# Kernel optimization log

Measured on AMD Instinct MI355X. Metric: run time of the kernel, lower is better.

Reference implementation:

```python
import jax, jax.numpy as jnp
import numpy as np

NUM_NODES = 20000
NUM_EDGES = 65536
WIDTH = 64
EDGE_FEAT = 6
HIDDEN = 128


def setup_inputs() -> dict:
    key = jax.random.key(0)
    ks = jax.random.split(key, 6)
    x = jax.random.normal(ks[0], (NUM_NODES, WIDTH), dtype=jnp.float32)
    edge_attr = jax.random.normal(ks[1], (NUM_EDGES, EDGE_FEAT), dtype=jnp.float32)
    # weight-generating MLP params (the `nn` callable), fan-in scaled
    W1 = jax.random.normal(ks[2], (EDGE_FEAT, HIDDEN), dtype=jnp.float32) / np.sqrt(EDGE_FEAT)
    b1 = jnp.zeros((HIDDEN,), dtype=jnp.float32)
    W2 = jax.random.normal(ks[3], (HIDDEN, WIDTH * WIDTH), dtype=jnp.float32) / np.sqrt(HIDDEN)
    b2 = jnp.zeros((WIDTH * WIDTH,), dtype=jnp.float32)
    senders = jax.random.randint(ks[4], (NUM_EDGES,), 0, NUM_NODES)
    receivers = jax.random.randint(ks[5], (NUM_EDGES,), 0, NUM_NODES)
    return {"x": x, "edge_attr": edge_attr, "W1": W1, "b1": b1,
            "W2": W2, "b2": b2, "senders": senders, "receivers": receivers}


def reference(x, edge_attr, W1, b1, W2, b2, senders, receivers):
    n_segs, width = x.shape
    # nn(edge_attr): (E, width*width) edge-conditioned weights
    h = jax.nn.relu(edge_attr @ W1 + b1)
    weight = (h @ W2 + b2).reshape(-1, width, width)  # (E, w, w)
    # gather sender features, per-edge (1,w) @ (w,w) matmul -> (E, w)
    msgs = jnp.einsum('ew,ewv->ev', x[senders], weight)
    # scatter-sum messages into receiver nodes (aggr == 'sum')
    return jax.ops.segment_sum(msgs, receivers, num_segments=n_segs)
```

## Files before the change

### kernel.cpp

```cpp
#include <hip/hip_runtime.h>
#include <stdint.h>

typedef _Float16 f16;
typedef f16 f16x8 __attribute__((ext_vector_type(8)));
typedef float f32x4 __attribute__((ext_vector_type(4)));

#define NUM_NODES 20000
#define NUM_EDGES 65536
#define WIDTH 64
#define EDGE_FEAT 6
#define HIDDEN 128
#define BM 256
#define NCHUNK 129
#define XPAD 72

#define XH_HALFS (NUM_NODES * WIDTH)
#define XCONV_BLKS 625
#define W2G_HALFS (NCHUNK * 4096)
#define HT_HALFS ((size_t)NCHUNK * NUM_EDGES)
#define HBLKS (NUM_EDGES / 256)
#define OUT_FLOATS (NUM_NODES * WIDTH)
#define ZBLKS 313

__device__ __forceinline__ void gload_lds16(const f16* g, f16* l) {
  __builtin_amdgcn_global_load_lds(
      (const __attribute__((address_space(1))) unsigned int*)g,
      (__attribute__((address_space(3))) unsigned int*)l, 16, 0, 0);
}

__global__ __launch_bounds__(256) void prep_kernel(
    const float* __restrict__ x, const float* __restrict__ W2,
    const float* __restrict__ b2, const float* __restrict__ ea,
    const float* __restrict__ W1, const float* __restrict__ b1,
    f16* __restrict__ ws_h, float* __restrict__ out, int use_ht)
{
  f16* x_h = ws_h;
  f16* W2g = ws_h + XH_HALFS;
  f16* hT  = ws_h + XH_HALFS + W2G_HALFS;
  const int blk = blockIdx.x, tid = threadIdx.x;

  if (blk < NCHUNK) {
    __shared__ float row[4096];
    const int ki = blk;
    const float* srcrow;
    if (ki < HIDDEN) {
      const float4* src = (const float4*)(W2 + (size_t)ki * 4096);
      #pragma unroll
      for (int i = 0; i < 4; ++i) {
        float4 v = src[tid + 256 * i];
        *(float4*)&row[(tid + 256 * i) * 4] = v;
      }
      __syncthreads();
      srcrow = row;
    } else {
      srcrow = b2;
    }
    const int obase = tid * 16;
    f16x8 outv0, outv1;
    #pragma unroll
    for (int u = 0; u < 8; ++u) {
      int o = obase + u;
      int n = o >> 6, pg = (o >> 3) & 7, j = o & 7;
      int k = (pg ^ (n & 7)) * 8 + j;
      outv0[u] = (f16)srcrow[k * 64 + n];
    }
    #pragma unroll
    for (int u = 0; u < 8; ++u) {
      int o = obase + 8 + u;
      int n = o >> 6, pg = (o >> 3) & 7, j = o & 7;
      int k = (pg ^ (n & 7)) * 8 + j;
      outv1[u] = (f16)srcrow[k * 64 + n];
    }
    *(f16x8*)&W2g[(size_t)ki * 4096 + obase] = outv0;
    *(f16x8*)&W2g[(size_t)ki * 4096 + obase + 8] = outv1;
  } else if (blk < NCHUNK + XCONV_BLKS) {
    int idx = (blk - NCHUNK) * 2048 + tid * 8;
    if (idx + 8 <= XH_HALFS) {
      float4 a = *(const float4*)(x + idx);
      float4 b = *(const float4*)(x + idx + 4);
      f16x8 hv;
      hv[0] = (f16)a.x; hv[1] = (f16)a.y; hv[2] = (f16)a.z; hv[3] = (f16)a.w;
      hv[4] = (f16)b.x; hv[5] = (f16)b.y; hv[6] = (f16)b.z; hv[7] = (f16)b.w;
      *(f16x8*)&x_h[idx] = hv;
    }
  } else if (blk < NCHUNK + XCONV_BLKS + ZBLKS) {
    int base = (blk - NCHUNK - XCONV_BLKS) * 4096 + tid * 16;
    float4 z = {0.f, 0.f, 0.f, 0.f};
    #pragma unroll
    for (int i = 0; i < 4; ++i) {
      int idx = base + i * 4;
      if (idx + 4 <= OUT_FLOATS) *(float4*)(out + idx) = z;
    }
  } else if (use_ht) {
    __shared__ float w1s[EDGE_FEAT * HIDDEN];
    __shared__ float b1s[HIDDEN];
    for (int i = tid; i < EDGE_FEAT * HIDDEN; i += 256) w1s[i] = W1[i];
    if (tid < HIDDEN) b1s[tid] = b1[tid];
    __syncthreads();
    const int e = (blk - NCHUNK - XCONV_BLKS - ZBLKS) * 256 + tid;
    const float* p = ea + (size_t)e * EDGE_FEAT;
    float a[6];
    #pragma unroll
    for (int f = 0; f < 6; ++f) a[f] = p[f];
    #pragma unroll 4
    for (int k = 0; k < HIDDEN; ++k) {
      float s = b1s[k];
      #pragma unroll
      for (int f = 0; f < 6; ++f) s = fmaf(a[f], w1s[f * HIDDEN + k], s);
      hT[(size_t)k * NUM_EDGES + e] = (f16)fmaxf(s, 0.f);
    }
    hT[(size_t)HIDDEN * NUM_EDGES + e] = (f16)1.f;
  }
}

template<int HT>
__global__ __launch_bounds__(256, 2) void nnconv_kernel(
    const float* __restrict__ ea, const float* __restrict__ W1,
    const float* __restrict__ b1, const int* __restrict__ senders,
    const int* __restrict__ receivers, const f16* __restrict__ ws_h,
    float* __restrict__ out)
{
  const f16* x_h = ws_h;
  const f16* W2g = ws_h + XH_HALFS;
  const f16* hT  = ws_h + XH_HALFS + W2G_HALFS;
  __shared__ __align__(16) f16 xt[BM][XPAD];
  __shared__ __align__(16) f16 Bb[2][4096];

  const int tid = threadIdx.x;
  const int lane = tid & 63, wid = tid >> 6;
  const int quad = lane >> 4, l15 = lane & 15;
  const int chunk = blockIdx.x & 255;
  const int khalf = blockIdx.x >> 8;
  const int k0 = khalf ? 65 : 0;
  const int kcount = khalf ? 64 : 65;
  const int e0 = chunk * BM;
  const int rowbase = wid * 64;

  {
    int s = senders[e0 + tid];
    const uint4* src = (const uint4*)(x_h + (size_t)s * WIDTH);
    uint4* dst = (uint4*)&xt[tid][0];
    #pragma unroll
    for (int i = 0; i < 8; ++i) dst[i] = src[i];
  }

  float ear[4][6];
  if (!HT) {
    #pragma unroll
    for (int t = 0; t < 4; ++t) {
      const float* p = ea + (size_t)(e0 + rowbase + t * 16 + l15) * EDGE_FEAT;
      #pragma unroll
      for (int f = 0; f < 6; ++f) ear[t][f] = p[f];
    }
  }

  int boff[2][4];
  #pragma unroll
  for (int kc = 0; kc < 2; ++kc)
    #pragma unroll
    for (int nt = 0; nt < 4; ++nt) {
      int n = nt * 16 + l15;
      int g = kc * 4 + quad;
      boff[kc][nt] = n * 64 + (g ^ (n & 7)) * 8;
    }

  const int hrow = e0 + rowbase + l15;
  const int stg_src = wid * 512 + (lane << 3);
  const int stg_dst = wid * 512;

  gload_lds16(W2g + (size_t)k0 * 4096 + stg_src, &Bb[0][stg_dst]);
  gload_lds16(W2g + (size_t)k0 * 4096 + 2048 + stg_src, &Bb[0][stg_dst + 2048]);
  f16 hc[4];
  if (HT) {
    const f16* hp = hT + (size_t)k0 * NUM_EDGES + hrow;
    #pragma unroll
    for (int t = 0; t < 4; ++t) hc[t] = hp[t * 16];
  }

  __syncthreads();

  f16x8 xf[4][2];
  #pragma unroll
  for (int t = 0; t < 4; ++t)
    #pragma unroll
    for (int kc = 0; kc < 2; ++kc)
      xf[t][kc] = *(const f16x8*)&xt[rowbase + t * 16 + l15][kc * 32 + quad * 8];

  f32x4 acc[4][4];
  #pragma unroll
  for (int t = 0; t < 4; ++t)
    #pragma unroll
    for (int nt = 0; nt < 4; ++nt)
      acc[t][nt] = (f32x4){0.f, 0.f, 0.f, 0.f};

  for (int kk = 0; kk < kcount; ++kk) {
    const int ki = k0 + kk;
    const int kin = (kk + 1 < kcount) ? ki + 1 : ki;
    f16* buf = &Bb[kk & 1][0];
    f16* nbuf = &Bb[(kk + 1) & 1][0];

    {
      const f16* src = W2g + (size_t)kin * 4096 + stg_src;
      gload_lds16(src, nbuf + stg_dst);
      gload_lds16(src + 2048, nbuf + stg_dst + 2048);
    }
    f16 hn[4];
    if (HT) {
      const f16* hp = hT + (size_t)kin * NUM_EDGES + hrow;
      #pragma unroll
      for (int t = 0; t < 4; ++t) hn[t] = hp[t * 16];
    }

    f16 hv[4];
    if (HT) {
      #pragma unroll
      for (int t = 0; t < 4; ++t) hv[t] = hc[t];
    } else {
      if (ki < HIDDEN) {
        float b1c = b1[ki];
        float w1c[6];
        #pragma unroll
        for (int f = 0; f < 6; ++f) w1c[f] = W1[f * HIDDEN + ki];
        #pragma unroll
        for (int t = 0; t < 4; ++t) {
          float s = b1c;
          #pragma unroll
          for (int f = 0; f < 6; ++f) s = fmaf(ear[t][f], w1c[f], s);
          hv[t] = (f16)fmaxf(s, 0.f);
        }
      } else {
        #pragma unroll
        for (int t = 0; t < 4; ++t) hv[t] = (f16)1.f;
      }
    }

    f16x8 bf[2][4];
    #pragma unroll
    for (int kc = 0; kc < 2; ++kc)
      #pragma unroll
      for (int nt = 0; nt < 4; ++nt)
        bf[kc][nt] = *(const f16x8*)&buf[boff[kc][nt]];

    #pragma unroll
    for (int t = 0; t < 4; ++t) {
      f16x8 sa0 = xf[t][0] * hv[t];
      f16x8 sa1 = xf[t][1] * hv[t];
      #pragma unroll
      for (int nt = 0; nt < 4; ++nt) {
        acc[t][nt] = __builtin_amdgcn_mfma_f32_16x16x32_f16(sa0, bf[0][nt], acc[t][nt], 0, 0, 0);
        acc[t][nt] = __builtin_amdgcn_mfma_f32_16x16x32_f16(sa1, bf[1][nt], acc[t][nt], 0, 0, 0);
      }
    }

    __builtin_amdgcn_sched_barrier(0);
    asm volatile("s_waitcnt vmcnt(0)" ::: "memory");
    asm volatile("s_barrier" ::: "memory");
    __builtin_amdgcn_sched_barrier(0);

    if (HT) {
      #pragma unroll
      for (int t = 0; t < 4; ++t) hc[t] = hn[t];
    }
  }

  #pragma unroll
  for (int t = 0; t < 4; ++t) {
    int ebase = e0 + rowbase + t * 16 + quad * 4;
    int rc[4];
    #pragma unroll
    for (int r = 0; r < 4; ++r) rc[r] = receivers[ebase + r];
    #pragma unroll
    for (int nt = 0; nt < 4; ++nt) {
      int v = nt * 16 + l15;
      #pragma unroll
      for (int r = 0; r < 4; ++r)
        atomicAdd(out + (size_t)rc[r] * WIDTH + v, acc[t][nt][r]);
    }
  }
}

extern "C" void kernel_launch(void* const* d_in, const int* in_sizes, int n_in,
                              void* d_out, int out_size, void* d_ws, size_t ws_size,
                              hipStream_t stream) {
  const float* x  = (const float*)d_in[0];
  const float* ea = (const float*)d_in[1];
  const float* W1 = (const float*)d_in[2];
  const float* b1 = (const float*)d_in[3];
  const float* W2 = (const float*)d_in[4];
  const float* b2 = (const float*)d_in[5];
  const int* snd  = (const int*)d_in[6];
  const int* rcv  = (const int*)d_in[7];
  float* out = (float*)d_out;
  f16* wsh = (f16*)d_ws;

  const size_t need = ((size_t)XH_HALFS + W2G_HALFS + HT_HALFS) * sizeof(f16);
  const int use_ht = (ws_size >= need) ? 1 : 0;

  const int prep_grid = NCHUNK + XCONV_BLKS + ZBLKS + (use_ht ? HBLKS : 0);
  prep_kernel<<<prep_grid, 256, 0, stream>>>(x, W2, b2, ea, W1, b1, wsh, out, use_ht);
  if (use_ht)
    nnconv_kernel<1><<<2 * (NUM_EDGES / BM), 256, 0, stream>>>(ea, W1, b1, snd, rcv, wsh, out);
  else
    nnconv_kernel<0><<<2 * (NUM_EDGES / BM), 256, 0, stream>>>(ea, W1, b1, snd, rcv, wsh, out);
}
```

Baseline: 169.3 us.

## Drop K-split, use one block per edge chunk with deeper register-prefetched pipeline

Removes the two-way split of the hidden dimension across blocks, so each of 256 blocks runs the full 129-step K loop and issues half as many atomic adds to the output. The loop is unrolled by two with B fragments double-buffered in registers, W2 chunks prefetched two steps ahead, and one combined waitcnt/barrier per step. This cuts atomic traffic and redundant x gathers, but the grid shrinks to 256 blocks (about one per CU on MI355X) with launch bounds relaxed to 1 block per CU, leaving less parallelism to hide latency.

```diff
diff --git a/kernel.cpp b/kernel.cpp
--- a/kernel.cpp
+++ b/kernel.cpp
@@ -114,7 +114,7 @@
 }
 
 template<int HT>
-__global__ __launch_bounds__(256, 2) void nnconv_kernel(
+__global__ __launch_bounds__(256, 1) void nnconv_kernel(
     const float* __restrict__ ea, const float* __restrict__ W1,
     const float* __restrict__ b1, const int* __restrict__ senders,
     const int* __restrict__ receivers, const f16* __restrict__ ws_h,
@@ -129,11 +129,7 @@
   const int tid = threadIdx.x;
   const int lane = tid & 63, wid = tid >> 6;
   const int quad = lane >> 4, l15 = lane & 15;
-  const int chunk = blockIdx.x & 255;
-  const int khalf = blockIdx.x >> 8;
-  const int k0 = khalf ? 65 : 0;
-  const int kcount = khalf ? 64 : 65;
-  const int e0 = chunk * BM;
+  const int e0 = blockIdx.x * BM;
   const int rowbase = wid * 64;
 
   {
@@ -168,13 +164,16 @@
   const int stg_src = wid * 512 + (lane << 3);
   const int stg_dst = wid * 512;
 
-  gload_lds16(W2g + (size_t)k0 * 4096 + stg_src, &Bb[0][stg_dst]);
-  gload_lds16(W2g + (size_t)k0 * 4096 + 2048 + stg_src, &Bb[0][stg_dst + 2048]);
-  f16 hc[4];
+  gload_lds16(W2g + stg_src, &Bb[0][stg_dst]);
+  gload_lds16(W2g + 2048 + stg_src, &Bb[0][stg_dst + 2048]);
+  gload_lds16(W2g + 4096 + stg_src, &Bb[1][stg_dst]);
+  gload_lds16(W2g + 4096 + 2048 + stg_src, &Bb[1][stg_dst + 2048]);
+  f16 hA[4], hB[4], hC[4];
   if (HT) {
-    const f16* hp = hT + (size_t)k0 * NUM_EDGES + hrow;
-    #pragma unroll
-    for (int t = 0; t < 4; ++t) hc[t] = hp[t * 16];
+    const f16* h0 = hT + hrow;
+    const f16* h1 = hT + (size_t)NUM_EDGES + hrow;
+    #pragma unroll
+    for (int t = 0; t < 4; ++t) { hA[t] = h0[t * 16]; hB[t] = h1[t * 16]; }
   }
 
   __syncthreads();
@@ -193,75 +192,78 @@
     for (int nt = 0; nt < 4; ++nt)
       acc[t][nt] = (f32x4){0.f, 0.f, 0.f, 0.f};
 
-  for (int kk = 0; kk < kcount; ++kk) {
-    const int ki = k0 + kk;
-    const int kin = (kk + 1 < kcount) ? ki + 1 : ki;
-    f16* buf = &Bb[kk & 1][0];
-    f16* nbuf = &Bb[(kk + 1) & 1][0];
-
-    {
-      const f16* src = W2g + (size_t)kin * 4096 + stg_src;
-      gload_lds16(src, nbuf + stg_dst);
-      gload_lds16(src + 2048, nbuf + stg_dst + 2048);
-    }
-    f16 hn[4];
-    if (HT) {
-      const f16* hp = hT + (size_t)kin * NUM_EDGES + hrow;
-      #pragma unroll
-      for (int t = 0; t < 4; ++t) hn[t] = hp[t * 16];
-    }
-
-    f16 hv[4];
-    if (HT) {
-      #pragma unroll
-      for (int t = 0; t < 4; ++t) hv[t] = hc[t];
-    } else {
-      if (ki < HIDDEN) {
-        float b1c = b1[ki];
-        float w1c[6];
-        #pragma unroll
-        for (int f = 0; f < 6; ++f) w1c[f] = W1[f * HIDDEN + ki];
-        #pragma unroll
-        for (int t = 0; t < 4; ++t) {
-          float s = b1c;
-          #pragma unroll
-          for (int f = 0; f < 6; ++f) s = fmaf(ear[t][f], w1c[f], s);
-          hv[t] = (f16)fmaxf(s, 0.f);
-        }
-      } else {
-        #pragma unroll
-        for (int t = 0; t < 4; ++t) hv[t] = (f16)1.f;
-      }
-    }
-
-    f16x8 bf[2][4];
-    #pragma unroll
-    for (int kc = 0; kc < 2; ++kc)
-      #pragma unroll
-      for (int nt = 0; nt < 4; ++nt)
-        bf[kc][nt] = *(const f16x8*)&buf[boff[kc][nt]];
-
-    #pragma unroll
-    for (int t = 0; t < 4; ++t) {
-      f16x8 sa0 = xf[t][0] * hv[t];
-      f16x8 sa1 = xf[t][1] * hv[t];
-      #pragma unroll
-      for (int nt = 0; nt < 4; ++nt) {
-        acc[t][nt] = __builtin_amdgcn_mfma_f32_16x16x32_f16(sa0, bf[0][nt], acc[t][nt], 0, 0, 0);
-        acc[t][nt] = __builtin_amdgcn_mfma_f32_16x16x32_f16(sa1, bf[1][nt], acc[t][nt], 0, 0, 0);
-      }
-    }
-
-    __builtin_amdgcn_sched_barrier(0);
-    asm volatile("s_waitcnt vmcnt(0)" ::: "memory");
-    asm volatile("s_barrier" ::: "memory");
-    __builtin_amdgcn_sched_barrier(0);
-
-    if (HT) {
-      #pragma unroll
-      for (int t = 0; t < 4; ++t) hc[t] = hn[t];
-    }
-  }
+  f16x8 bfA[2][4], bfB[2][4];
+  #pragma unroll
+  for (int kc = 0; kc < 2; ++kc)
+    #pragma unroll
+    for (int nt = 0; nt < 4; ++nt)
+      bfA[kc][nt] = *(const f16x8*)&Bb[0][boff[kc][nt]];
+
+#define NN_STEP(K, CUR, NXT, DOREAD)                                          \
+  {                                                                           \
+    asm volatile("s_waitcnt vmcnt(%0) lgkmcnt(0)\n\ts_barrier"                \
+                 :: "i"(HT ? 4 : 0) : "memory");                              \
+    const int c2_ = ((K) + 2 <= 128) ? (K) + 2 : 128;                         \
+    {                                                                         \
+      const f16* src_ = W2g + (size_t)c2_ * 4096 + stg_src;                   \
+      f16* dst_ = &Bb[(K) & 1][stg_dst];                                      \
+      gload_lds16(src_, dst_);                                                \
+      gload_lds16(src_ + 2048, dst_ + 2048);                                  \
+    }                                                                         \
+    __builtin_amdgcn_sched_barrier(0);      \
+    if (HT) {                                                                 \
+      const f16* hp_ = hT + (size_t)c2_ * NUM_EDGES + hrow;                   \
+      hC[0] = hp_[0]; hC[1] = hp_[16]; hC[2] = hp_[32]; hC[3] = hp_[48];      \
+    }                                                                         \
+    if (DOREAD) {                                                             \
+      f16* rb_ = &Bb[((K) + 1) & 1][0];                                       \
+      _Pragma("unroll") for (int kc = 0; kc < 2; ++kc)                        \
+        _Pragma("unroll") for (int nt = 0; nt < 4; ++nt)                      \
+          NXT[kc][nt] = *(const f16x8*)&rb_[boff[kc][nt]];                    \
+    }                                                                         \
+    f16 hv_[4];                                                               \
+    if (HT) {                                                                 \
+      _Pragma("unroll") for (int t = 0; t < 4; ++t) hv_[t] = hA[t];           \
+    } else {                                                                  \
+      if ((K) < HIDDEN) {                                                     \
+        float b1c_ = b1[(K)];                                                 \
+        float w1c_[6];                                                        \
+        _Pragma("unroll") for (int f = 0; f < 6; ++f)                         \
+          w1c_[f] = W1[f * HIDDEN + (K)];                                     \
+        _Pragma("unroll") for (int t = 0; t < 4; ++t) {                       \
+          float s_ = b1c_;                                                    \
+          _Pragma("unroll") for (int f = 0; f < 6; ++f)                       \
+            s_ = fmaf(ear[t][f], w1c_[f], s_);                                \
+          hv_[t] = (f16)fmaxf(s_, 0.f);                                       \
+        }                                                                     \
+      } else {                                                                \
+        _Pragma("unroll") for (int t = 0; t < 4; ++t) hv_[t] = (f16)1.f;      \
+      }                                                                       \
+    }                                                                         \
+    _Pragma("unroll") for (int t = 0; t < 4; ++t) {                           \
+      f16x8 sa0_ = xf[t][0] * hv_[t];                                         \
+      f16x8 sa1_ = xf[t][1] * hv_[t];                                         \
+      _Pragma("unroll") for (int nt = 0; nt < 4; ++nt) {                      \
+        acc[t][nt] = __builtin_amdgcn_mfma_f32_16x16x32_f16(                  \
+            sa0_, CUR[0][nt], acc[t][nt], 0, 0, 0);                           \
+        acc[t][nt] = __builtin_amdgcn_mfma_f32_16x16x32_f16(                  \
+            sa1_, CUR[1][nt], acc[t][nt], 0, 0, 0);                           \
+      }                                                                       \
+    }                                                                         \
+    if (HT) {                                                                 \
+      _Pragma("unroll") for (int t = 0; t < 4; ++t) {                         \
+        hA[t] = hB[t]; hB[t] = hC[t];                                         \
+      }                                                                       \
+    }                                                                         \
+  }
+
+  #pragma unroll 1
+  for (int kb = 0; kb < 64; ++kb) {
+    NN_STEP(2 * kb,     bfA, bfB, true);
+    NN_STEP(2 * kb + 1, bfB, bfA, true);
+  }
+  NN_STEP(128, bfA, bfB, false);
+#undef NN_STEP
 
   #pragma unroll
   for (int t = 0; t < 4; ++t) {
@@ -299,7 +301,7 @@
   const int prep_grid = NCHUNK + XCONV_BLKS + ZBLKS + (use_ht ? HBLKS : 0);
   prep_kernel<<<prep_grid, 256, 0, stream>>>(x, W2, b2, ea, W1, b1, wsh, out, use_ht);
   if (use_ht)
-    nnconv_kernel<1><<<2 * (NUM_EDGES / BM), 256, 0, stream>>>(ea, W1, b1, snd, rcv, wsh, out);
+    nnconv_kernel<1><<<NUM_EDGES / BM, 256, 0, stream>>>(ea, W1, b1, snd, rcv, wsh, out);
   else
-    nnconv_kernel<0><<<2 * (NUM_EDGES / BM), 256, 0, stream>>>(ea, W1, b1, snd, rcv, wsh, out);
+    nnconv_kernel<0><<<NUM_EDGES / BM, 256, 0, stream>>>(ea, W1, b1, snd, rcv, wsh, out);
 }
```

Result: slower. 175.6 us (+3.7%).
